# Kernel optimization log

Measured on AMD Instinct MI355X. Metric: run time of the kernel, lower is better.

The kernel has to match this reference:

```python
import jax, jax.numpy as jnp
import numpy as np

B = 131072
IN_DIM = 100
H = 256


def setup_inputs() -> dict:
    key = jax.random.key(0)
    ks = jax.random.split(key, 7)
    return {
        "x": jax.random.normal(ks[0], (B, IN_DIM), dtype=jnp.float32),
        "C": jax.random.normal(ks[1], (B, H), dtype=jnp.float32),
        "h": jax.random.normal(ks[2], (B, H), dtype=jnp.float32),
        # stacked gate weights, gate order: i, f, g, o  (equivalent to 8 separate Linears)
        "Wx": jax.random.normal(ks[3], (IN_DIM, 4 * H), dtype=jnp.float32) * 0.05,
        "Wh": jax.random.normal(ks[4], (H, 4 * H), dtype=jnp.float32) * 0.05,
        "bx": jax.random.normal(ks[5], (4 * H,), dtype=jnp.float32) * 0.05,
        "bh": jax.random.normal(ks[6], (4 * H,), dtype=jnp.float32) * 0.05,
    }


def reference(x, C, h, Wx, Wh, bx, bh):
    # two fused GEMMs replace the 8 per-gate Linears (same math)
    gates = (x @ Wx + bx) + (h @ Wh + bh)  # [B, 4H]
    i_pre, f_pre, g_pre, o_pre = jnp.split(gates, 4, axis=-1)
    i = jax.nn.sigmoid(i_pre)
    f = jax.nn.sigmoid(f_pre)
    g = jnp.tanh(g_pre)
    o = jax.nn.sigmoid(o_pre)
    c_out = f * C + i * g
    h_out = o * jnp.tanh(c_out)
    return (c_out, h_out)
```

## Files before the change

### kernel.cpp

```cpp
#include <hip/hip_runtime.h>
#include <stdint.h>


typedef short bf16x8 __attribute__((ext_vector_type(8)));
typedef float f32x4  __attribute__((ext_vector_type(4)));

#define HDIM   256
#define INDIM  100
#define NROWS  131072
#define BT_OFF 0
#define XB_OFF (1048576 / 2)
#define HB_OFF (35651584 / 2)
#define ABUF(b) ((b) * 8192)
#define BBUF(b) (24576 + (b) * 8192)

__device__ __forceinline__ float fexp(float x) {
  return __builtin_amdgcn_exp2f(x * 1.44269504088896340736f);
}
__device__ __forceinline__ float frcp(float x) { return __builtin_amdgcn_rcpf(x); }
__device__ __forceinline__ float sigm(float x) { return frcp(1.0f + fexp(-x)); }
__device__ __forceinline__ float tanh_fast(float x) {
  return 1.0f - 2.0f * frcp(1.0f + fexp(2.0f * x));
}
__device__ __forceinline__ unsigned short f2bf_rne(float f) {
  union { float f; uint32_t u; } v; v.f = f;
  return (unsigned short)((v.u + 0x7FFFu + ((v.u >> 16) & 1u)) >> 16);
}
__device__ __forceinline__ void gl16(const void* g, void* l) {
  __builtin_amdgcn_global_load_lds(
      (const __attribute__((address_space(1))) unsigned int*)g,
      (__attribute__((address_space(3))) unsigned int*)l, 16, 0, 0);
}
#define VMW(N) asm volatile("s_waitcnt vmcnt(" #N ")" ::: "memory")

__global__ void prep_all(const float* __restrict__ X, const float* __restrict__ Hin,
                         const float* __restrict__ Wx, const float* __restrict__ Wh,
                         const float* __restrict__ bxp, const float* __restrict__ bhp,
                         unsigned short* __restrict__ ws) {
  const int b = blockIdx.x, tid = threadIdx.x;
  if (b < 8192) {
    const int t   = b * 256 + tid;
    const int row = t >> 4, k0 = (t & 15) * 8;
    const float* xp = X + (size_t)row * INDIM;
    float4 lo = make_float4(0.f, 0.f, 0.f, 0.f);
    float4 hi = make_float4(0.f, 0.f, 0.f, 0.f);
    if (k0 + 4 <= INDIM) lo = *reinterpret_cast<const float4*>(xp + k0);
    if (k0 + 8 <= INDIM) hi = *reinterpret_cast<const float4*>(xp + k0 + 4);
    float va[8] = {lo.x, lo.y, lo.z, lo.w, hi.x, hi.y, hi.z, hi.w};
    unsigned short o[8];
#pragma unroll
    for (int e = 0; e < 8; ++e) {
      const int k = k0 + e;
      const float f = (k < INDIM) ? va[e] : (k == 127 ? 1.0f : 0.0f);
      o[e] = f2bf_rne(f);
    }
    *reinterpret_cast<bf16x8*>(ws + XB_OFF + (size_t)row * 128 + k0) =
        *reinterpret_cast<bf16x8*>(o);
  } else if (b < 24576) {
    const int t   = (b - 8192) * 256 + tid;
    const int row = t >> 5, k0 = (t & 31) * 8;
    const float* hp = Hin + (size_t)row * HDIM + k0;
    const float4 lo = *reinterpret_cast<const float4*>(hp);
    const float4 hi = *reinterpret_cast<const float4*>(hp + 4);
    unsigned short o[8] = {f2bf_rne(lo.x), f2bf_rne(lo.y), f2bf_rne(lo.z),
                           f2bf_rne(lo.w), f2bf_rne(hi.x), f2bf_rne(hi.y),
                           f2bf_rne(hi.z), f2bf_rne(hi.w)};
    *reinterpret_cast<bf16x8*>(ws + HB_OFF + (size_t)row * 256 + k0) =
        *reinterpret_cast<bf16x8*>(o);
  } else {
    const int unit = (b - 24576) * 4 + (tid >> 6);
    const int lane = tid & 63;
    const int kst  = unit % 12;
    const int fidb = unit / 12;
    const int bn   = fidb >> 3, fid = fidb & 7;
    const int g    = fid >> 1,  wc  = fid & 1;
    const int wcol = g * HDIM + bn * 32 + wc * 16 + (lane & 15);
    const int kb   = kst * 32 + (lane >> 4) * 8;
    unsigned short v[8];
#pragma unroll
    for (int e = 0; e < 8; ++e) {
      const int k = kb + e;
      float f = 0.0f;
      if (k < INDIM)     f = Wx[(size_t)k * 1024 + wcol];
      else if (k == 127) f = bxp[wcol] + bhp[wcol];
      else if (k >= 128) f = Wh[(size_t)(k - 128) * 1024 + wcol];
      v[e] = f2bf_rne(f);
    }
    *reinterpret_cast<bf16x8*>(ws + BT_OFF + (size_t)unit * 512 + lane * 8) =
        *reinterpret_cast<bf16x8*>(v);
  }
}

__global__ __launch_bounds__(256, 3)
void lstm_main(const unsigned short* __restrict__ ws,
               const float* __restrict__ Cin, float* __restrict__ out)
{
  __shared__ unsigned char smem[49152];

  const int tid  = threadIdx.x;
  const int orig = blockIdx.x;
  const int lg   = ((orig & 7) << 10) | (orig >> 3);
  const int mt   = lg >> 3;
  const int bn   = lg & 7;

  const int lane = tid & 63;
  const int l15  = lane & 15;
  const int kq   = lane >> 4;
  const int wid  = tid >> 6;
  const int wr   = wid >> 1;
  const int wc   = wid & 1;
  const int ch   = bn * 32 + wc * 16 + l15;
  const int sx   = (l15 >> 1) & 3;

  const unsigned short* xb = ws + XB_OFF;
  const unsigned short* hb = ws + HB_OFF;
  const unsigned short* Bt = ws + BT_OFF;

  const unsigned short* xsrc[2];
  const unsigned short* hsrc[2];
  const unsigned short* bsrc[2];
#pragma unroll
  for (int j = 0; j < 2; ++j) {
    const int ci  = (wid * 2 + j) * 64 + lane;
    const int r   = ci >> 2;
    const int sc  = (ci & 3) ^ ((r >> 1) & 3);
    xsrc[j] = xb + (size_t)(mt * 128 + r) * 128 + sc * 8;
    hsrc[j] = hb + (size_t)(mt * 128 + r) * 256 + sc * 8;
    bsrc[j] = Bt + (size_t)((bn * 8 + wid * 2 + j) * 12) * 512 + lane * 8;
  }
  const int au0 = (wid * 2 + 0) * 1024;
  const int au1 = (wid * 2 + 1) * 1024;

  f32x4 acc[4][4];
#pragma unroll
  for (int m = 0; m < 4; ++m)
#pragma unroll
    for (int g = 0; g < 4; ++g)
#pragma unroll
      for (int e = 0; e < 4; ++e) acc[m][g][e] = 0.0f;

  float cvv[4][4];

  auto STAGE = [&](int T) {
    char* Ad = (char*)smem + ABUF(T % 3);
    char* Bd = (char*)smem + BBUF(T % 3);
    if (T < 4) {
      gl16(xsrc[0] + T * 32, Ad + au0);
      gl16(xsrc[1] + T * 32, Ad + au1);
    } else {
      gl16(hsrc[0] + (T - 4) * 32, Ad + au0);
      gl16(hsrc[1] + (T - 4) * 32, Ad + au1);
    }
    gl16(bsrc[0] + T * 512, Bd + au0);
    gl16(bsrc[1] + T * 512, Bd + au1);
  };

  auto COMPUTE = [&](int S) {
    const unsigned short* Ab = (const unsigned short*)(smem + ABUF(S % 3));
    const unsigned short* Bb = (const unsigned short*)(smem + BBUF(S % 3));
    bf16x8 afr[4], bfr[4];
#pragma unroll
    for (int m = 0; m < 4; ++m)
      afr[m] = *reinterpret_cast<const bf16x8*>(
          Ab + (wr * 64 + m * 16 + l15) * 32 + ((kq ^ sx) * 8));
#pragma unroll
    for (int g = 0; g < 4; ++g)
      bfr[g] = *reinterpret_cast<const bf16x8*>(
          Bb + (g * 2 + wc) * 512 + lane * 8);
    __builtin_amdgcn_s_setprio(1);
#pragma unroll
    for (int m = 0; m < 4; ++m)
#pragma unroll
      for (int g = 0; g < 4; ++g)
        acc[m][g] = __builtin_amdgcn_mfma_f32_16x16x32_bf16(
            afr[m], bfr[g], acc[m][g], 0, 0, 0);
    __builtin_amdgcn_s_setprio(0);
  };

  STAGE(0);
  STAGE(1);

#define STEP(S, KN)                                               \
  do {                                                            \
    VMW(KN);                                                      \
    __builtin_amdgcn_s_barrier();                                 \
    if ((S) + 2 < 12) STAGE((S) + 2);                             \
    if ((S) == 9) {                                               \
      const float* cb =                                           \
          Cin + ((size_t)mt * 128 + wr * 64 + kq * 4) * HDIM + ch;\
      _Pragma("unroll")                                           \
      for (int m = 0; m < 4; ++m)                                 \
        _Pragma("unroll")                                         \
        for (int e = 0; e < 4; ++e)                               \
          cvv[m][e] = cb[(size_t)(m * 16 + e) * HDIM];            \
    }                                                             \
    COMPUTE(S);                                                   \
  } while (0)

  STEP(0, 4);  STEP(1, 4);  STEP(2, 4);  STEP(3, 4);
  STEP(4, 4);  STEP(5, 4);  STEP(6, 4);  STEP(7, 4);
  STEP(8, 4);  STEP(9, 4);  STEP(10, 12); STEP(11, 8);
#undef STEP

  float* op  = out + ((size_t)mt * 128 + wr * 64 + kq * 4) * HDIM + ch;
  float* op2 = op + (size_t)NROWS * HDIM;
#pragma unroll
  for (int m = 0; m < 4; ++m) {
#pragma unroll
    for (int e = 0; e < 4; ++e) {
      const float pi = acc[m][0][e];
      const float pf = acc[m][1][e];
      const float pg = acc[m][2][e];
      const float po = acc[m][3][e];
      const float ig = sigm(pi), fg = sigm(pf);
      const float gg = tanh_fast(pg), og = sigm(po);
      const float co = fg * cvv[m][e] + ig * gg;
      const float ho = og * tanh_fast(co);
      op [(size_t)(m * 16 + e) * HDIM] = co;
      op2[(size_t)(m * 16 + e) * HDIM] = ho;
    }
  }
}

extern "C" void kernel_launch(void* const* d_in, const int* in_sizes, int n_in,
                              void* d_out, int out_size, void* d_ws, size_t ws_size,
                              hipStream_t stream) {
  const float* x  = (const float*)d_in[0];
  const float* C  = (const float*)d_in[1];
  const float* h  = (const float*)d_in[2];
  const float* Wx = (const float*)d_in[3];
  const float* Wh = (const float*)d_in[4];
  const float* bx = (const float*)d_in[5];
  const float* bh = (const float*)d_in[6];
  float* o = (float*)d_out;
  unsigned short* ws = (unsigned short*)d_ws;

  prep_all<<<dim3(24768), dim3(256), 0, stream>>>(x, h, Wx, Wh, bx, bh, ws);
  lstm_main<<<dim3(8192), dim3(256), 0, stream>>>(ws, C, o);
}
```

Baseline: 213.7 us.

## Widen main-kernel tile to 128x64 channels with 512-thread blocks

Doubles the output-channel width per block (64 hidden channels, 8 waves) so each staged A tile of x/h rows is reused across twice as many gate columns. This halves the number of times the activation rows are re-read from global memory, at the cost of larger LDS (72KB) and lower block occupancy. It also adjusts the vmcnt waits for the new per-stage load count and switches the C loads and output stores to nontemporal hints so they bypass the cache.

```diff
diff --git a/kernel.cpp b/kernel.cpp
--- a/kernel.cpp
+++ b/kernel.cpp
@@ -12,7 +12,7 @@
 #define XB_OFF (1048576 / 2)
 #define HB_OFF (35651584 / 2)
 #define ABUF(b) ((b) * 8192)
-#define BBUF(b) (24576 + (b) * 8192)
+#define BBUF(b) (24576 + (b) * 16384)
 
 __device__ __forceinline__ float fexp(float x) {
   return __builtin_amdgcn_exp2f(x * 1.44269504088896340736f);
@@ -91,45 +91,47 @@
   }
 }
 
-__global__ __launch_bounds__(256, 3)
+__global__ __launch_bounds__(512, 2)
 void lstm_main(const unsigned short* __restrict__ ws,
                const float* __restrict__ Cin, float* __restrict__ out)
 {
-  __shared__ unsigned char smem[49152];
+  __shared__ unsigned char smem[73728];
 
   const int tid  = threadIdx.x;
   const int orig = blockIdx.x;
-  const int lg   = ((orig & 7) << 10) | (orig >> 3);
-  const int mt   = lg >> 3;
-  const int bn   = lg & 7;
+  const int lg   = ((orig & 7) << 9) | (orig >> 3);
+  const int mt   = lg >> 2;
+  const int bnn  = lg & 3;
 
   const int lane = tid & 63;
   const int l15  = lane & 15;
   const int kq   = lane >> 4;
   const int wid  = tid >> 6;
-  const int wr   = wid >> 1;
-  const int wc   = wid & 1;
-  const int ch   = bn * 32 + wc * 16 + l15;
+  const int wr   = wid >> 2;
+  const int wcq  = wid & 3;
+  const int ch   = bnn * 64 + wcq * 16 + l15;
   const int sx   = (l15 >> 1) & 3;
 
   const unsigned short* xb = ws + XB_OFF;
   const unsigned short* hb = ws + HB_OFF;
   const unsigned short* Bt = ws + BT_OFF;
 
-  const unsigned short* xsrc[2];
-  const unsigned short* hsrc[2];
+  const int ci = wid * 64 + lane;
+  const int r  = ci >> 2;
+  const int sc = (ci & 3) ^ ((r >> 1) & 3);
+  const unsigned short* xsrc = xb + (size_t)(mt * 128 + r) * 128 + sc * 8;
+  const unsigned short* hsrc = hb + (size_t)(mt * 128 + r) * 256 + sc * 8;
+
   const unsigned short* bsrc[2];
 #pragma unroll
   for (int j = 0; j < 2; ++j) {
-    const int ci  = (wid * 2 + j) * 64 + lane;
-    const int r   = ci >> 2;
-    const int sc  = (ci & 3) ^ ((r >> 1) & 3);
-    xsrc[j] = xb + (size_t)(mt * 128 + r) * 128 + sc * 8;
-    hsrc[j] = hb + (size_t)(mt * 128 + r) * 256 + sc * 8;
-    bsrc[j] = Bt + (size_t)((bn * 8 + wid * 2 + j) * 12) * 512 + lane * 8;
+    const int u  = wid * 2 + j;
+    const int gu = (bnn * 2 + (u >> 3)) * 8 + (u & 7);
+    bsrc[j] = Bt + (size_t)gu * 12 * 512 + lane * 8;
   }
-  const int au0 = (wid * 2 + 0) * 1024;
-  const int au1 = (wid * 2 + 1) * 1024;
+  const int adst = wid * 1024;
+  const int bd0  = (wid * 2 + 0) * 1024;
+  const int bd1  = (wid * 2 + 1) * 1024;
 
   f32x4 acc[4][4];
 #pragma unroll
@@ -144,15 +146,10 @@
   auto STAGE = [&](int T) {
     char* Ad = (char*)smem + ABUF(T % 3);
     char* Bd = (char*)smem + BBUF(T % 3);
-    if (T < 4) {
-      gl16(xsrc[0] + T * 32, Ad + au0);
-      gl16(xsrc[1] + T * 32, Ad + au1);
-    } else {
-      gl16(hsrc[0] + (T - 4) * 32, Ad + au0);
-      gl16(hsrc[1] + (T - 4) * 32, Ad + au1);
-    }
-    gl16(bsrc[0] + T * 512, Bd + au0);
-    gl16(bsrc[1] + T * 512, Bd + au1);
+    if (T < 4) gl16(xsrc + T * 32, Ad + adst);
+    else       gl16(hsrc + (T - 4) * 32, Ad + adst);
+    gl16(bsrc[0] + T * 512, Bd + bd0);
+    gl16(bsrc[1] + T * 512, Bd + bd1);
   };
 
   auto COMPUTE = [&](int S) {
@@ -164,9 +161,10 @@
       afr[m] = *reinterpret_cast<const bf16x8*>(
           Ab + (wr * 64 + m * 16 + l15) * 32 + ((kq ^ sx) * 8));
 #pragma unroll
-    for (int g = 0; g < 4; ++g)
-      bfr[g] = *reinterpret_cast<const bf16x8*>(
-          Bb + (g * 2 + wc) * 512 + lane * 8);
+    for (int g = 0; g < 4; ++g) {
+      const int ub = (wcq >> 1) * 8 + g * 2 + (wcq & 1);
+      bfr[g] = *reinterpret_cast<const bf16x8*>(Bb + ub * 512 + lane * 8);
+    }
     __builtin_amdgcn_s_setprio(1);
 #pragma unroll
     for (int m = 0; m < 4; ++m)
@@ -192,15 +190,18 @@
       for (int m = 0; m < 4; ++m)                                 \
         _Pragma("unroll")                                         \
         for (int e = 0; e < 4; ++e)                               \
-          cvv[m][e] = cb[(size_t)(m * 16 + e) * HDIM];            \
+          cvv[m][e] = __builtin_nontemporal_load(                 \
+              cb + (size_t)(m * 16 + e) * HDIM);                  \
     }                                                             \
     COMPUTE(S);                                                   \
   } while (0)
 
-  STEP(0, 4);  STEP(1, 4);  STEP(2, 4);  STEP(3, 4);
-  STEP(4, 4);  STEP(5, 4);  STEP(6, 4);  STEP(7, 4);
-  STEP(8, 4);  STEP(9, 4);  STEP(10, 12); STEP(11, 8);
+  STEP(0, 3);  STEP(1, 3);  STEP(2, 3);  STEP(3, 3);
+  STEP(4, 3);  STEP(5, 3);  STEP(6, 3);  STEP(7, 3);
+  STEP(8, 3);  STEP(9, 3);  STEP(10, 19); STEP(11, 16);
 #undef STEP
+
+  VMW(0);
 
   float* op  = out + ((size_t)mt * 128 + wr * 64 + kq * 4) * HDIM + ch;
   float* op2 = op + (size_t)NROWS * HDIM;
@@ -216,8 +217,8 @@
       const float gg = tanh_fast(pg), og = sigm(po);
       const float co = fg * cvv[m][e] + ig * gg;
       const float ho = og * tanh_fast(co);
-      op [(size_t)(m * 16 + e) * HDIM] = co;
-      op2[(size_t)(m * 16 + e) * HDIM] = ho;
+      __builtin_nontemporal_store(co, op  + (size_t)(m * 16 + e) * HDIM);
+      __builtin_nontemporal_store(ho, op2 + (size_t)(m * 16 + e) * HDIM);
     }
   }
 }
@@ -236,5 +237,5 @@
   unsigned short* ws = (unsigned short*)d_ws;
 
   prep_all<<<dim3(24768), dim3(256), 0, stream>>>(x, h, Wx, Wh, bx, bh, ws);
-  lstm_main<<<dim3(8192), dim3(256), 0, stream>>>(ws, C, o);
-}
+  lstm_main<<<dim3(4096), dim3(512), 0, stream>>>(ws, C, o);
+}
```

New measurement: 195.6 us. 8.5% less time.

## Give each wave private LDS buffers to drop block barriers in GEMM pipeline

Applied to the files above, without the earlier changes.

Each wave now stages its own A and B tiles into a private double-buffered LDS region instead of sharing a triple-buffered block-wide region. This lets the per-step s_barrier be removed, with compute issued before the next prefetch. Each wave loads twice as many chunks, so A and B rows are fetched redundantly across waves and LDS grows to 64KB, which cuts occupancy from 3 to 2 blocks per CU. C loads and output stores also become nontemporal.

```diff
diff --git a/kernel.cpp b/kernel.cpp
--- a/kernel.cpp
+++ b/kernel.cpp
@@ -11,8 +11,6 @@
 #define BT_OFF 0
 #define XB_OFF (1048576 / 2)
 #define HB_OFF (35651584 / 2)
-#define ABUF(b) ((b) * 8192)
-#define BBUF(b) (24576 + (b) * 8192)
 
 __device__ __forceinline__ float fexp(float x) {
   return __builtin_amdgcn_exp2f(x * 1.44269504088896340736f);
@@ -91,11 +89,11 @@
   }
 }
 
-__global__ __launch_bounds__(256, 3)
+__global__ __launch_bounds__(256, 2)
 void lstm_main(const unsigned short* __restrict__ ws,
                const float* __restrict__ Cin, float* __restrict__ out)
 {
-  __shared__ unsigned char smem[49152];
+  __shared__ unsigned char smem[65536];
 
   const int tid  = threadIdx.x;
   const int orig = blockIdx.x;
@@ -116,20 +114,21 @@
   const unsigned short* hb = ws + HB_OFF;
   const unsigned short* Bt = ws + BT_OFF;
 
-  const unsigned short* xsrc[2];
-  const unsigned short* hsrc[2];
-  const unsigned short* bsrc[2];
-#pragma unroll
-  for (int j = 0; j < 2; ++j) {
-    const int ci  = (wid * 2 + j) * 64 + lane;
-    const int r   = ci >> 2;
-    const int sc  = (ci & 3) ^ ((r >> 1) & 3);
-    xsrc[j] = xb + (size_t)(mt * 128 + r) * 128 + sc * 8;
-    hsrc[j] = hb + (size_t)(mt * 128 + r) * 256 + sc * 8;
-    bsrc[j] = Bt + (size_t)((bn * 8 + wid * 2 + j) * 12) * 512 + lane * 8;
+  char* const wls = (char*)smem + wid * 16384;
+
+  const unsigned short* xsrc[4];
+  const unsigned short* hsrc[4];
+  const unsigned short* bsrc[4];
+#pragma unroll
+  for (int j = 0; j < 4; ++j) {
+    const int cj = j * 64 + lane;
+    const int r  = cj >> 2;
+    const int sc = (cj & 3) ^ ((r >> 1) & 3);
+    const int gr = mt * 128 + wr * 64 + r;
+    xsrc[j] = xb + (size_t)gr * 128 + sc * 8;
+    hsrc[j] = hb + (size_t)gr * 256 + sc * 8;
+    bsrc[j] = Bt + (size_t)((bn * 8 + j * 2 + wc) * 12) * 512 + lane * 8;
   }
-  const int au0 = (wid * 2 + 0) * 1024;
-  const int au1 = (wid * 2 + 1) * 1024;
 
   f32x4 acc[4][4];
 #pragma unroll
@@ -142,31 +141,31 @@
   float cvv[4][4];
 
   auto STAGE = [&](int T) {
-    char* Ad = (char*)smem + ABUF(T % 3);
-    char* Bd = (char*)smem + BBUF(T % 3);
+    char* Ad = wls + (T & 1) * 4096;
+    char* Bd = wls + 8192 + (T & 1) * 4096;
     if (T < 4) {
-      gl16(xsrc[0] + T * 32, Ad + au0);
-      gl16(xsrc[1] + T * 32, Ad + au1);
+#pragma unroll
+      for (int j = 0; j < 4; ++j) gl16(xsrc[j] + T * 32, Ad + j * 1024);
     } else {
-      gl16(hsrc[0] + (T - 4) * 32, Ad + au0);
-      gl16(hsrc[1] + (T - 4) * 32, Ad + au1);
-    }
-    gl16(bsrc[0] + T * 512, Bd + au0);
-    gl16(bsrc[1] + T * 512, Bd + au1);
+#pragma unroll
+      for (int j = 0; j < 4; ++j) gl16(hsrc[j] + (T - 4) * 32, Ad + j * 1024);
+    }
+#pragma unroll
+    for (int g = 0; g < 4; ++g) gl16(bsrc[g] + T * 512, Bd + g * 1024);
   };
 
   auto COMPUTE = [&](int S) {
-    const unsigned short* Ab = (const unsigned short*)(smem + ABUF(S % 3));
-    const unsigned short* Bb = (const unsigned short*)(smem + BBUF(S % 3));
+    const unsigned short* Ab = (const unsigned short*)(wls + (S & 1) * 4096);
+    const unsigned short* Bb =
+        (const unsigned short*)(wls + 8192 + (S & 1) * 4096);
     bf16x8 afr[4], bfr[4];
 #pragma unroll
     for (int m = 0; m < 4; ++m)
       afr[m] = *reinterpret_cast<const bf16x8*>(
-          Ab + (wr * 64 + m * 16 + l15) * 32 + ((kq ^ sx) * 8));
+          Ab + (m * 16 + l15) * 32 + ((kq ^ sx) * 8));
 #pragma unroll
     for (int g = 0; g < 4; ++g)
-      bfr[g] = *reinterpret_cast<const bf16x8*>(
-          Bb + (g * 2 + wc) * 512 + lane * 8);
+      bfr[g] = *reinterpret_cast<const bf16x8*>(Bb + g * 512 + lane * 8);
     __builtin_amdgcn_s_setprio(1);
 #pragma unroll
     for (int m = 0; m < 4; ++m)
@@ -183,7 +182,7 @@
 #define STEP(S, KN)                                               \
   do {                                                            \
     VMW(KN);                                                      \
-    __builtin_amdgcn_s_barrier();                                 \
+    COMPUTE(S);                                                   \
     if ((S) + 2 < 12) STAGE((S) + 2);                             \
     if ((S) == 9) {                                               \
       const float* cb =                                           \
@@ -192,15 +191,17 @@
       for (int m = 0; m < 4; ++m)                                 \
         _Pragma("unroll")                                         \
         for (int e = 0; e < 4; ++e)                               \
-          cvv[m][e] = cb[(size_t)(m * 16 + e) * HDIM];            \
+          cvv[m][e] = __builtin_nontemporal_load(                 \
+              cb + (size_t)(m * 16 + e) * HDIM);                  \
     }                                                             \
-    COMPUTE(S);                                                   \
   } while (0)
 
-  STEP(0, 4);  STEP(1, 4);  STEP(2, 4);  STEP(3, 4);
-  STEP(4, 4);  STEP(5, 4);  STEP(6, 4);  STEP(7, 4);
-  STEP(8, 4);  STEP(9, 4);  STEP(10, 12); STEP(11, 8);
+  STEP(0, 8);  STEP(1, 8);  STEP(2, 8);  STEP(3, 8);
+  STEP(4, 8);  STEP(5, 8);  STEP(6, 8);  STEP(7, 8);
+  STEP(8, 8);  STEP(9, 8);  STEP(10, 24); STEP(11, 16);
 #undef STEP
+
+  VMW(0);
 
   float* op  = out + ((size_t)mt * 128 + wr * 64 + kq * 4) * HDIM + ch;
   float* op2 = op + (size_t)NROWS * HDIM;
@@ -216,8 +217,8 @@
       const float gg = tanh_fast(pg), og = sigm(po);
       const float co = fg * cvv[m][e] + ig * gg;
       const float ho = og * tanh_fast(co);
-      op [(size_t)(m * 16 + e) * HDIM] = co;
-      op2[(size_t)(m * 16 + e) * HDIM] = ho;
+      __builtin_nontemporal_store(co, op  + (size_t)(m * 16 + e) * HDIM);
+      __builtin_nontemporal_store(ho, op2 + (size_t)(m * 16 + e) * HDIM);
     }
   }
 }
```

Measured after the change: 248.4 us. 16.2% more time.
